# Kernel tuning notes

Measured on AMD Instinct MI355X. Metric: run time of the kernel, lower is better.

The kernel has to match this reference:

```python
import jax, jax.numpy as jnp
import numpy as np

N_NODES = 6890
N_ANGLES = 8
K_CHEB = 15
N_DESC = 544
HIDDEN = 64
N_CLASS = 6890
M = N_ANGLES * N_NODES  # 55120, size of anisotropic Laplacian
DEG = 16
NNZ = M * DEG
BN_EPS = 1e-5


def setup_inputs() -> dict:
    key = jax.random.key(0)
    ks = jax.random.split(key, 16)
    x = jax.random.normal(ks[0], (N_NODES, N_DESC), dtype=jnp.float32)
    # sparse anisotropic Laplacian (M x M), ~DEG nnz per row
    rows = jnp.repeat(jnp.arange(M, dtype=jnp.int32), DEG)
    cols = jax.random.randint(ks[1], (NNZ,), 0, M, dtype=jnp.int32)
    vals = jax.random.normal(ks[2], (NNZ,), dtype=jnp.float32) * 0.1
    # conv1: (K, n_angles*n_desc, 64); conv2..6 stacked: (5, K, n_angles*64, 64)
    def xavier(k, shape, fan_in, fan_out):
        lim = np.sqrt(6.0 / (fan_in + fan_out))
        return jax.random.uniform(k, shape, jnp.float32, -lim, lim)
    W1 = xavier(ks[3], (K_CHEB, N_ANGLES * N_DESC, HIDDEN), N_ANGLES * N_DESC, HIDDEN)
    Wc = xavier(ks[4], (5, K_CHEB, N_ANGLES * HIDDEN, HIDDEN), N_ANGLES * HIDDEN, HIDDEN)
    conv_b = jnp.zeros((6, HIDDEN), jnp.float32)
    bn_gamma = jnp.ones((6, HIDDEN), jnp.float32)
    bn_beta = jnp.zeros((6, HIDDEN), jnp.float32)
    fc2_w = xavier(ks[5], (HIDDEN, 256), HIDDEN, 256)
    fc2_b = jnp.zeros((256,), jnp.float32)
    fc3_w = xavier(ks[6], (256, N_CLASS), 256, N_CLASS)
    fc3_b = jnp.zeros((N_CLASS,), jnp.float32)
    return {"x": x, "rows": rows, "cols": cols, "vals": vals,
            "W1": W1, "Wc": Wc, "conv_b": conv_b,
            "bn_gamma": bn_gamma, "bn_beta": bn_beta,
            "fc2_w": fc2_w, "fc2_b": fc2_b, "fc3_w": fc3_w, "fc3_b": fc3_b}


def _spmm(rows, cols, vals, T):
    # (M x M sparse) @ (M x C) via gather + segment-sum
    return jax.ops.segment_sum(vals[:, None] * T[cols], rows, num_segments=M)


def _acs_conv(x, rows, cols, vals, W, b):
    # x: (N, C). Chebyshev recurrence on the (A*N, C) angle-stacked signal.
    N, C = x.shape
    A = N_ANGLES

    def proj(T, Wk):
        # (A*N, C) -> (N, A*C) @ (A*C, out)
        return T.reshape(A, N, C).transpose(1, 0, 2).reshape(N, A * C) @ Wk

    T0 = jnp.tile(x, (A, 1))
    out = proj(T0, W[0])
    T1 = _spmm(rows, cols, vals, T0)
    out = out + proj(T1, W[1])
    for k in range(2, K_CHEB):
        T2 = 2.0 * _spmm(rows, cols, vals, T1) - T0
        out = out + proj(T2, W[k])
        T0, T1 = T1, T2
    return out + b


def _bn_relu(x, gamma, beta):
    # BatchNorm1d (training-mode batch stats, biased variance) + ReLU
    mean = jnp.mean(x, axis=0)
    var = jnp.var(x, axis=0)
    return jax.nn.relu((x - mean) * jax.lax.rsqrt(var + BN_EPS) * gamma + beta)


def reference(x, rows, cols, vals, W1, Wc, conv_b, bn_gamma, bn_beta,
              fc2_w, fc2_b, fc3_w, fc3_b):
    h = _bn_relu(_acs_conv(x, rows, cols, vals, W1, conv_b[0]), bn_gamma[0], bn_beta[0])
    for i in range(5):
        h = _bn_relu(_acs_conv(h, rows, cols, vals, Wc[i], conv_b[i + 1]),
                     bn_gamma[i + 1], bn_beta[i + 1])
    h = jax.nn.relu(h @ fc2_w + fc2_b)
    # dropout is identity at inference
    return h @ fc3_w + fc3_b
```

## Files before the change

### kernel.cpp

```cpp
#include <hip/hip_runtime.h>
#include <cstdint>
#include <cstddef>

#define NN 6890
#define NA 8
#define KC 15
#define ND 544
#define MR (NA * NN)
#define DEG 16
#define NNZ (MR * DEG)
#define BN_EPS 1e-5f
#define NRG 108
#define PB (NA * NRG)

typedef unsigned int u32;
typedef _Float16 f16;
typedef __attribute__((ext_vector_type(8))) _Float16 f16x8;
typedef __attribute__((ext_vector_type(4))) float f32x4;

union U4H8 { uint4 q; f16 h[8]; f16x8 v; };

__device__ __forceinline__ u32 packh(float a, float b) {
    union { f16 h[2]; u32 u; } c;
    c.h[0] = (f16)a; c.h[1] = (f16)b; return c.u;
}
__device__ __forceinline__ uint4 pack8h(const float* t) {
    uint4 m;
    m.x = packh(t[0], t[1]); m.y = packh(t[2], t[3]);
    m.z = packh(t[4], t[5]); m.w = packh(t[6], t[7]);
    return m;
}
__device__ __forceinline__ void acc8h(float* s, float v, uint4 g) {
    U4H8 c; c.q = g;
    #pragma unroll
    for (int i = 0; i < 8; ++i) s[i] += v * (float)c.h[i];
}

__global__ __launch_bounds__(256)
void prep_cv_kernel(const int* __restrict__ cols, const float* __restrict__ vals,
                    uint4* __restrict__ cvq)
{
    const int q = blockIdx.x * 256 + threadIdx.x;
    if (q >= NNZ / 4) return;
    const int4   c = ((const int4*)cols)[q];
    const float4 v = ((const float4*)vals)[q];
    uint4 o;
    o.x = ((u32)c.x & 0xffffu) | ((u32)c.y << 16);
    o.y = ((u32)c.z & 0xffffu) | ((u32)c.w << 16);
    o.z = packh(v.x, v.y);
    o.w = packh(v.z, v.w);
    cvq[q] = o;
}

template<int CC>
__global__ __launch_bounds__(256)
void tile_slab_kernel(const float* __restrict__ X, int C_in, int c0,
                      uint4* __restrict__ slab0)
{
    constexpr int LPR = CC / 8;
    constexpr int RPB = 256 / LPR;
    const int tid = threadIdx.x;
    const int j = tid % LPR, rloc = tid / LPR;
    const int r = blockIdx.x * RPB + rloc;
    if (r >= MR) return;
    const int n = r % NN;
    const float* xp = X + (size_t)n * C_in + c0 + 8 * j;
    const float4 t0 = *(const float4*)xp;
    const float4 t1 = *(const float4*)(xp + 4);
    float t[8] = { t0.x, t0.y, t0.z, t0.w, t1.x, t1.y, t1.z, t1.w };
    slab0[(size_t)r * LPR + j] = pack8h(t);
}

template<int CC, bool CHEB>
__device__ __forceinline__
void spmm_body(const uint4* __restrict__ sp, const uint4* __restrict__ sc,
               uint4* __restrict__ sw, const uint4* __restrict__ cvq,
               uint4* cvl)
{
    constexpr int LPR = CC / 8;
    constexpr int RPB = 256 / LPR;
    const int tid = threadIdx.x;
    const int j = tid % LPR, rloc = tid / LPR;
    const int r0 = blockIdx.x * RPB;
    const int nrow = (MR - r0) < RPB ? (MR - r0) : RPB;
    for (int e = tid; e < nrow * 4; e += 256)
        cvl[e] = cvq[(size_t)r0 * 4 + e];
    __syncthreads();
    const int r = r0 + rloc;
    if (r >= MR) return;

    int c[16]; float v[16];
    #pragma unroll
    for (int q = 0; q < 4; ++q) {
        const uint4 cq = cvl[rloc * 4 + q];
        c[4 * q + 0] = cq.x & 0xffffu; c[4 * q + 1] = cq.x >> 16;
        c[4 * q + 2] = cq.y & 0xffffu; c[4 * q + 3] = cq.y >> 16;
        union { u32 u; f16 h[2]; } z, w_;
        z.u = cq.z; w_.u = cq.w;
        v[4 * q + 0] = (float)z.h[0]; v[4 * q + 1] = (float)z.h[1];
        v[4 * q + 2] = (float)w_.h[0]; v[4 * q + 3] = (float)w_.h[1];
    }
    float s[8] = {0.f, 0.f, 0.f, 0.f, 0.f, 0.f, 0.f, 0.f};
    #pragma unroll
    for (int d = 0; d < DEG; ++d)
        acc8h(s, v[d], sp[(size_t)c[d] * LPR + j]);
    float t[8];
    if (CHEB) {
        U4H8 p; p.q = sc[(size_t)r * LPR + j];
        #pragma unroll
        for (int i = 0; i < 8; ++i) t[i] = 2.f * s[i] - (float)p.h[i];
    } else {
        #pragma unroll
        for (int i = 0; i < 8; ++i) t[i] = s[i];
    }
    sw[(size_t)r * LPR + j] = pack8h(t);
}

template<int CC, bool CHEB>
__global__ __launch_bounds__(256)
void spmm_only_kernel(const uint4* __restrict__ sp, const uint4* __restrict__ sc,
                      uint4* __restrict__ sw, const uint4* __restrict__ cvq)
{
    constexpr int RPB = 256 / (CC / 8);
    __shared__ uint4 cvl[RPB * 4];
    spmm_body<CC, CHEB>(sp, sc, sw, cvq, cvl);
}

template<int SCC, int NPROJ, bool FIRSTP>
__device__ __forceinline__
void proj_body(int pb, const uint4* __restrict__ s0, const uint4* __restrict__ s1,
               const float* __restrict__ W, float* __restrict__ part,
               int C_in, int c0, int kbase, u32* WH, u32* WL)
{
    constexpr int LPRF   = SCC / 8;
    constexpr int SLICES = SCC >= 64 ? SCC / 64 : 1;
    constexpr int SCH    = SCC >= 64 ? 64 : SCC;
    constexpr int CCH    = SCH / 32;
    const int tid = threadIdx.x;
    const int l = tid & 63, w = tid >> 6;
    const int a = pb / NRG, rg = pb % NRG;
    const int rows0 = rg * 64;
    const int hi16 = l >> 4;

    const int arow = rows0 + w * 16 + (l & 15);
    const int arc  = arow < NN ? arow : NN - 1;
    const size_t abase = (size_t)(a * NN + arc) * LPRF;

    f32x4 acc[4];
    #pragma unroll
    for (int nt = 0; nt < 4; ++nt) {
        #pragma unroll
        for (int rr = 0; rr < 4; ++rr) {
            const int orow = rows0 + w * 16 + hi16 * 4 + rr;
            float vv = 0.f;
            if (!FIRSTP && orow < NN)
                vv = part[((size_t)a * NN + orow) * 64 + nt * 16 + (l & 15)];
            acc[nt][rr] = vv;
        }
    }

    #pragma unroll
    for (int p = 0; p < NPROJ; ++p) {
        const uint4* sl = (p == 0) ? s0 : s1;
        #pragma unroll
        for (int s = 0; s < SLICES; ++s) {
            const float* Wk = W + ((size_t)(kbase + p) * NA * C_in
                                   + (size_t)a * C_in + c0 + s * 64) * 64;
            if (p | s) __syncthreads();
            for (int e = tid; e < CCH * 1024; e += 256) {
                const int i2 = e & 3;
                const int ll = (e >> 2) & 63;
                const int nt = (e >> 8) & 3;
                const int h  = e >> 10;
                const int cc  = h * 32 + (ll >> 4) * 8 + 2 * i2;
                const int col = nt * 16 + (ll & 15);
                const float w0 = Wk[(size_t)cc * 64 + col];
                const float w1 = Wk[(size_t)(cc + 1) * 64 + col];
                const f16 h0 = (f16)w0, h1 = (f16)w1;
                union { f16 h[2]; u32 u; } ph, pl;
                ph.h[0] = h0; ph.h[1] = h1;
                pl.h[0] = (f16)(w0 - (float)h0); pl.h[1] = (f16)(w1 - (float)h1);
                WH[e] = ph.u; WL[e] = pl.u;
            }
            __syncthreads();
            #pragma unroll
            for (int h = 0; h < CCH; ++h) {
                U4H8 af; af.q = sl[abase + s * 8 + h * 4 + hi16];
                #pragma unroll
                for (int nt = 0; nt < 4; ++nt) {
                    const int be = ((h * 4 + nt) * 64 + l) * 4;
                    U4H8 bh, bl;
                    bh.q = *(const uint4*)&WH[be];
                    bl.q = *(const uint4*)&WL[be];
                    acc[nt] = __builtin_amdgcn_mfma_f32_16x16x32_f16(af.v, bh.v, acc[nt], 0, 0, 0);
                    acc[nt] = __builtin_amdgcn_mfma_f32_16x16x32_f16(af.v, bl.v, acc[nt], 0, 0, 0);
                }
            }
        }
    }

    #pragma unroll
    for (int nt = 0; nt < 4; ++nt) {
        #pragma unroll
        for (int rr = 0; rr < 4; ++rr) {
            const int orow = rows0 + w * 16 + hi16 * 4 + rr;
            if (orow < NN)
                part[((size_t)a * NN + orow) * 64 + nt * 16 + (l & 15)] = acc[nt][rr];
        }
    }
}

template<int CC, bool FIRSTP>
__global__ __launch_bounds__(256)
void step2_kernel(const uint4* __restrict__ sp, const uint4* __restrict__ sc,
                  uint4* __restrict__ sw, const uint4* __restrict__ cvq,
                  const float* __restrict__ W, float* __restrict__ part,
                  int C_in, int c0, int kbase, int NB)
{
    constexpr int RPB = 256 / (CC / 8);
    __shared__ uint4 cvl[RPB * 4];
    __shared__ u32 WH[2048];
    __shared__ u32 WL[2048];
    if ((int)blockIdx.x < NB)
        spmm_body<CC, true>(sp, sc, sw, cvq, cvl);
    else
        proj_body<CC, 2, FIRSTP>((int)blockIdx.x - NB, sc, sp, W, part, C_in, c0, kbase, WH, WL);
}

template<int CC>
__global__ __launch_bounds__(256)
void proj_final_kernel(const uint4* __restrict__ sl, const float* __restrict__ W,
                       float* __restrict__ part, int C_in, int c0, int kproj)
{
    __shared__ u32 WH[2048];
    __shared__ u32 WL[2048];
    proj_body<CC, 1, false>((int)blockIdx.x, sl, sl, W, part, C_in, c0, kproj, WH, WL);
}

__global__ void bn_reduce_kernel(const float* __restrict__ part, float* __restrict__ acc)
{
    const int e = blockIdx.x * blockDim.x + threadIdx.x;
    if (e >= NN * 64) return;
    float s = 0.f;
    #pragma unroll
    for (int a = 0; a < NA; ++a) s += part[(size_t)a * NN * 64 + e];
    acc[e] = s;
}

__global__ __launch_bounds__(256)
void bn_stats_kernel(const float* __restrict__ acc, const float* __restrict__ gamma,
                     const float* __restrict__ beta, float* __restrict__ bnp)
{
    const int h = blockIdx.x;
    float s = 0.f, sq = 0.f;
    for (int n = threadIdx.x; n < NN; n += 256) {
        const float v = acc[(size_t)n * 64 + h];
        s += v; sq += v * v;
    }
    __shared__ float ls[256], lq[256];
    ls[threadIdx.x] = s; lq[threadIdx.x] = sq;
    __syncthreads();
    for (int st = 128; st > 0; st >>= 1) {
        if (threadIdx.x < st) { ls[threadIdx.x] += ls[threadIdx.x + st]; lq[threadIdx.x] += lq[threadIdx.x + st]; }
        __syncthreads();
    }
    if (threadIdx.x == 0) {
        const float mean = ls[0] / (float)NN;
        const float var  = lq[0] / (float)NN - mean * mean;
        const float sc   = gamma[h] / sqrtf(var + BN_EPS);
        bnp[h]      = sc;
        bnp[64 + h] = beta[h] - mean * sc;
    }
}

__global__ void bn_apply_kernel(const float* __restrict__ acc, const float* __restrict__ bnp,
                                float* __restrict__ H)
{
    const int e = blockIdx.x * blockDim.x + threadIdx.x;
    if (e >= NN * 64) return;
    const int h = e & 63;
    const float v = acc[e] * bnp[h] + bnp[64 + h];
    H[e] = v > 0.f ? v : 0.f;
}

template<bool RELU>
__global__ __launch_bounds__(256)
void gemm_bias_kernel(const float* __restrict__ A, const float* __restrict__ B,
                      const float* __restrict__ bias, float* __restrict__ C,
                      int Mm, int Nn, int Kk)
{
    __shared__ float As[16][132];
    __shared__ float Bs[16][132];
    const int tx = threadIdx.x & 15, ty = threadIdx.x >> 4;
    const int m0 = blockIdx.y * 128, n0 = blockIdx.x * 128;
    const bool full = (m0 + 128 <= Mm) && (n0 + 128 <= Nn);
    float acc[8][8] = {};
    for (int k0 = 0; k0 < Kk; k0 += 16) {
        if (full) {
            #pragma unroll
            for (int e = threadIdx.x; e < 512; e += 256) {
                const int i = e >> 2, q = e & 3;
                const float4 a4 = *(const float4*)&A[(size_t)(m0 + i) * Kk + k0 + 4 * q];
                As[4 * q + 0][i] = a4.x; As[4 * q + 1][i] = a4.y;
                As[4 * q + 2][i] = a4.z; As[4 * q + 3][i] = a4.w;
            }
            #pragma unroll
            for (int e = threadIdx.x; e < 512; e += 256) {
                const int kk = e >> 5, q = e & 31;
                *(float4*)&Bs[kk][4 * q] = *(const float4*)&B[(size_t)(k0 + kk) * Nn + n0 + 4 * q];
            }
        } else {
            for (int e = threadIdx.x; e < 128 * 16; e += 256) {
                const int i = e >> 4, kk = e & 15;
                const int row = m0 + i;
                As[kk][i] = (row < Mm) ? A[(size_t)row * Kk + k0 + kk] : 0.f;
            }
            for (int e = threadIdx.x; e < 16 * 128; e += 256) {
                const int kk = e >> 7, jj = e & 127;
                const int col = n0 + jj;
                Bs[kk][jj] = (col < Nn) ? B[(size_t)(k0 + kk) * Nn + col] : 0.f;
            }
        }
        __syncthreads();
        #pragma unroll
        for (int kk = 0; kk < 16; ++kk) {
            float av[8], bv[8];
            *(float4*)&av[0] = *(const float4*)&As[kk][ty * 4];
            *(float4*)&av[4] = *(const float4*)&As[kk][64 + ty * 4];
            *(float4*)&bv[0] = *(const float4*)&Bs[kk][tx * 4];
            *(float4*)&bv[4] = *(const float4*)&Bs[kk][64 + tx * 4];
            #pragma unroll
            for (int i = 0; i < 8; ++i)
                #pragma unroll
                for (int jj = 0; jj < 8; ++jj)
                    acc[i][jj] += av[i] * bv[jj];
        }
        __syncthreads();
    }
    for (int i = 0; i < 8; ++i) {
        const int row = m0 + (i < 4 ? ty * 4 + i : 64 + ty * 4 + (i - 4));
        if (row >= Mm) continue;
        for (int jj = 0; jj < 8; ++jj) {
            const int col = n0 + (jj < 4 ? tx * 4 + jj : 64 + tx * 4 + (jj - 4));
            if (col >= Nn) continue;
            float v = acc[i][jj] + bias[col];
            if (RELU) v = fmaxf(v, 0.f);
            C[(size_t)row * Nn + col] = v;
        }
    }
}

__global__ __launch_bounds__(256)
void w3_split_kernel(const float* __restrict__ W, f16* __restrict__ Wh, f16* __restrict__ Wl)
{
    __shared__ float t[64][65];
    const int tid = threadIdx.x;
    const int n0 = blockIdx.x * 64, k0 = blockIdx.y * 64;
    for (int e = tid; e < 64 * 64; e += 256) {
        const int kk = e >> 6, nn = e & 63;
        const int gn = n0 + nn;
        t[kk][nn] = (gn < NN) ? W[(size_t)(k0 + kk) * NN + gn] : 0.f;
    }
    __syncthreads();
    for (int e = tid; e < 64 * 8; e += 256) {
        const int nn = e >> 3, c8 = e & 7;
        const int gn = n0 + nn;
        if (gn >= NN) continue;
        const size_t ob = ((size_t)((k0 >> 3) + c8) * NN + gn) * 8;
        f16 vh[8], vl[8];
        #pragma unroll
        for (int i = 0; i < 8; ++i) {
            const float w = t[c8 * 8 + i][nn];
            const f16 h = (f16)w;
            vh[i] = h; vl[i] = (f16)(w - (float)h);
        }
        *(uint4*)&Wh[ob] = *(const uint4*)vh;
        *(uint4*)&Wl[ob] = *(const uint4*)vl;
    }
}

__global__ __launch_bounds__(256)
void f2_split_kernel(const float* __restrict__ f2, f16* __restrict__ Ah, f16* __restrict__ Al)
{
    const int row = blockIdx.x * 256 + threadIdx.x;
    const int c = blockIdx.y;
    if (row >= NN) return;
    const float4 a0 = *(const float4*)&f2[(size_t)row * 256 + c * 8];
    const float4 a1 = *(const float4*)&f2[(size_t)row * 256 + c * 8 + 4];
    const float vv[8] = { a0.x, a0.y, a0.z, a0.w, a1.x, a1.y, a1.z, a1.w };
    f16 vh[8], vl[8];
    #pragma unroll
    for (int i = 0; i < 8; ++i) {
        const f16 h = (f16)vv[i];
        vh[i] = h; vl[i] = (f16)(vv[i] - (float)h);
    }
    const size_t ob = ((size_t)c * NN + row) * 8;
    *(uint4*)&Ah[ob] = *(const uint4*)vh;
    *(uint4*)&Al[ob] = *(const uint4*)vl;
}

__global__ __launch_bounds__(256)
void fc3_mfma_kernel(const f16* __restrict__ Ah, const f16* __restrict__ Al,
                     const f16* __restrict__ Bh, const f16* __restrict__ Bl,
                     const float* __restrict__ bias, float* __restrict__ C)
{
    const int tid = threadIdx.x, l = tid & 63, w = tid >> 6;
    const int wm = w >> 1, wn = w & 1, hi16 = l >> 4;
    const int m0 = blockIdx.y * 128, n0 = blockIdx.x * 128;

    size_t aoff[4], boff[4];
    #pragma unroll
    for (int mf = 0; mf < 4; ++mf) {
        int row = m0 + wm * 64 + mf * 16 + (l & 15);
        if (row > NN - 1) row = NN - 1;
        aoff[mf] = (size_t)row * 8;
    }
    #pragma unroll
    for (int nf = 0; nf < 4; ++nf) {
        int col = n0 + wn * 64 + nf * 16 + (l & 15);
        if (col > NN - 1) col = NN - 1;
        boff[nf] = (size_t)col * 8;
    }

    f32x4 acc[4][4];
    #pragma unroll
    for (int mf = 0; mf < 4; ++mf)
        #pragma unroll
        for (int nf = 0; nf < 4; ++nf)
            acc[mf][nf] = (f32x4){0.f, 0.f, 0.f, 0.f};

    for (int k0 = 0; k0 < 256; k0 += 32) {
        const size_t cb = (size_t)((k0 >> 3) + hi16) * NN * 8;
        f16x8 ah[4], al[4], bh[4], bl[4];
        #pragma unroll
        for (int mf = 0; mf < 4; ++mf) {
            ah[mf] = *(const f16x8*)(Ah + cb + aoff[mf]);
            al[mf] = *(const f16x8*)(Al + cb + aoff[mf]);
        }
        #pragma unroll
        for (int nf = 0; nf < 4; ++nf) {
            bh[nf] = *(const f16x8*)(Bh + cb + boff[nf]);
            bl[nf] = *(const f16x8*)(Bl + cb + boff[nf]);
        }
        #pragma unroll
        for (int mf = 0; mf < 4; ++mf)
            #pragma unroll
            for (int nf = 0; nf < 4; ++nf) {
                acc[mf][nf] = __builtin_amdgcn_mfma_f32_16x16x32_f16(ah[mf], bh[nf], acc[mf][nf], 0, 0, 0);
                acc[mf][nf] = __builtin_amdgcn_mfma_f32_16x16x32_f16(ah[mf], bl[nf], acc[mf][nf], 0, 0, 0);
                acc[mf][nf] = __builtin_amdgcn_mfma_f32_16x16x32_f16(al[mf], bh[nf], acc[mf][nf], 0, 0, 0);
            }
    }

    #pragma unroll
    for (int mf = 0; mf < 4; ++mf) {
        #pragma unroll
        for (int nf = 0; nf < 4; ++nf) {
            const int col = n0 + wn * 64 + nf * 16 + (l & 15);
            if (col >= NN) continue;
            const float bv = bias[col];
            #pragma unroll
            for (int rr = 0; rr < 4; ++rr) {
                const int row = m0 + wm * 64 + mf * 16 + hi16 * 4 + rr;
                if (row < NN)
                    C[(size_t)row * NN + col] = acc[mf][nf][rr] + bv;
            }
        }
    }
}

template<int CC>
static void run_chunk(bool first, const float* X, int C_in, int c0,
                      const uint4* cvq, const float* W,
                      uint4* slabs, float* part, hipStream_t stream)
{
    constexpr int RPB = 256 / (CC / 8);
    const int NB = (MR + RPB - 1) / RPB;
    const size_t SLOT = (size_t)MR * (CC / 8);
    uint4* sl[3] = { slabs, slabs + SLOT, slabs + 2 * SLOT };

    tile_slab_kernel<CC><<<NB, 256, 0, stream>>>(X, C_in, c0, sl[0]);
    spmm_only_kernel<CC, false><<<NB, 256, 0, stream>>>(sl[0], sl[0], sl[1], cvq);
    for (int k = 2; k < KC; ++k) {
        const int p = (k - 1) % 3, c = (k - 2) % 3, n = k % 3;
        if (k & 1) {
            spmm_only_kernel<CC, true><<<NB, 256, 0, stream>>>(sl[p], sl[c], sl[n], cvq);
        } else {
            if (first && k == 2)
                step2_kernel<CC, true ><<<NB + PB, 256, 0, stream>>>(
                    sl[p], sl[c], sl[n], cvq, W, part, C_in, c0, k - 2, NB);
            else
                step2_kernel<CC, false><<<NB + PB, 256, 0, stream>>>(
                    sl[p], sl[c], sl[n], cvq, W, part, C_in, c0, k - 2, NB);
        }
    }
    proj_final_kernel<CC><<<PB, 256, 0, stream>>>(sl[(KC - 1) % 3], W, part, C_in, c0, KC - 1);
}

extern "C" void kernel_launch(void* const* d_in, const int* in_sizes, int n_in,
                              void* d_out, int out_size, void* d_ws, size_t ws_size,
                              hipStream_t stream)
{
    (void)in_sizes; (void)n_in; (void)out_size;
    const float* x     = (const float*)d_in[0];
    const int*   cols  = (const int*)  d_in[2];
    const float* vals  = (const float*)d_in[3];
    const float* W1    = (const float*)d_in[4];
    const float* Wc    = (const float*)d_in[5];
    const float* gamma = (const float*)d_in[7];
    const float* beta  = (const float*)d_in[8];
    const float* fc2w  = (const float*)d_in[9];
    const float* fc2b  = (const float*)d_in[10];
    const float* fc3w  = (const float*)d_in[11];
    const float* fc3b  = (const float*)d_in[12];

    const size_t MT = (size_t)MR * 64;
    const size_t FIXED = (size_t)(NNZ / 4) * 16
                       + MT * 4
                       + (size_t)NN * 64 * 4 * 2
                       + (size_t)NN * 256 * 4
                       + (size_t)NN * 256 * 2 * 4
                       + 1024;
    const size_t ring256 = 3 * (size_t)MR * 512;
    const size_t ring128 = 3 * (size_t)MR * 256;
    const size_t ring64  = 3 * (size_t)MR * 128;
    int ccL0 = 64;
    size_t ring = ring64;
    if (ws_size >= FIXED + ring256)      { ccL0 = 256; ring = ring256; }
    else if (ws_size >= FIXED + ring128) { ccL0 = 128; ring = ring128; }

    char* base = (char*)d_ws;
    size_t off = 0;
    uint4* cvq  = (uint4*)(base + off); off += (size_t)(NNZ / 4) * 16;
    uint4* slabs = (uint4*)(base + off); off += ring;
    float* part = (float*)(base + off); off += MT * 4;
    float* acc  = (float*)(base + off); off += (size_t)NN * 64 * 4;
    float* H    = (float*)(base + off); off += (size_t)NN * 64 * 4;
    float* f2   = (float*)(base + off); off += (size_t)NN * 256 * 4;
    f16* f2h    = (f16*)(base + off);   off += (size_t)NN * 256 * 2;
    f16* f2l    = (f16*)(base + off);   off += (size_t)NN * 256 * 2;
    f16* W3h    = (f16*)(base + off);   off += (size_t)NN * 256 * 2;
    f16* W3l    = (f16*)(base + off);   off += (size_t)NN * 256 * 2;
    float* bnp  = (float*)(base + off);

    prep_cv_kernel<<<(NNZ / 4 + 255) / 256, 256, 0, stream>>>(cols, vals, cvq);
    w3_split_kernel<<<dim3(108, 4), 256, 0, stream>>>(fc3w, W3h, W3l);

    for (int li = 0; li < 6; ++li) {
        const int C_in = (li == 0) ? ND : 64;
        const float* X = (li == 0) ? x : H;
        const float* W = (li == 0) ? W1 : Wc + (size_t)(li - 1) * KC * (NA * 64) * 64;

        if (li == 0) {
            int c0 = 0;
            bool first = true;
            const int wide = ccL0;
            while (c0 + wide <= 512) {
                if (wide == 256)      run_chunk<256>(first, X, C_in, c0, cvq, W, slabs, part, stream);
                else if (wide == 128) run_chunk<128>(first, X, C_in, c0, cvq, W, slabs, part, stream);
                else                  run_chunk<64> (first, X, C_in, c0, cvq, W, slabs, part, stream);
                c0 += wide; first = false;
            }
            while (c0 + 64 <= ND) {
                run_chunk<64>(first, X, C_in, c0, cvq, W, slabs, part, stream);
                c0 += 64; first = false;
            }
            run_chunk<32>(false, X, C_in, c0, cvq, W, slabs, part, stream);
        } else {
            run_chunk<64>(true, X, C_in, 0, cvq, W, slabs, part, stream);
        }

        bn_reduce_kernel<<<(NN * 64 + 255) / 256, 256, 0, stream>>>(part, acc);
        bn_stats_kernel<<<64, 256, 0, stream>>>(acc, gamma + li * 64, beta + li * 64, bnp);
        bn_apply_kernel<<<(NN * 64 + 255) / 256, 256, 0, stream>>>(acc, bnp, H);
    }

    gemm_bias_kernel<true><<<dim3(2, 54), 256, 0, stream>>>(H, fc2w, fc2b, f2, NN, 256, 64);
    f2_split_kernel<<<dim3(27, 32), 256, 0, stream>>>(f2, f2h, f2l);
    fc3_mfma_kernel<<<dim3(54, 54), 256, 0, stream>>>(f2h, f2l, W3h, W3l, fc3b, (float*)d_out);
}
```

Baseline: 4.172 ms.

## Fuse BN-ReLU into slab tiling and use output buffer as slab ring

Applies the BatchNorm scale/shift and ReLU inside the slab-tiling kernel for layers 2-6, so the separate bn_apply pass runs only after the last layer. The Chebyshev slab ring now lives in the output buffer, which lets layer 1 always use 256-wide channel chunks (two 256 chunks plus a 32 remainder) regardless of workspace size. This removes one elementwise kernel and its memory traffic per layer and gives fewer, wider chunks in the first layer. It relies on the output buffer being large enough to hold the ring and being fully overwritten by the final fc3 kernel.

```diff
diff --git a/kernel.cpp b/kernel.cpp
--- a/kernel.cpp
+++ b/kernel.cpp
@@ -52,10 +52,10 @@
     cvq[q] = o;
 }
 
-template<int CC>
+template<int CC, bool BN>
 __global__ __launch_bounds__(256)
 void tile_slab_kernel(const float* __restrict__ X, int C_in, int c0,
-                      uint4* __restrict__ slab0)
+                      uint4* __restrict__ slab0, const float* __restrict__ bnp)
 {
     constexpr int LPR = CC / 8;
     constexpr int RPB = 256 / LPR;
@@ -68,6 +68,14 @@
     const float4 t0 = *(const float4*)xp;
     const float4 t1 = *(const float4*)(xp + 4);
     float t[8] = { t0.x, t0.y, t0.z, t0.w, t1.x, t1.y, t1.z, t1.w };
+    if (BN) {
+        const int ch = c0 + 8 * j;
+        #pragma unroll
+        for (int i = 0; i < 8; ++i) {
+            const float v = t[i] * bnp[ch + i] + bnp[64 + ch + i];
+            t[i] = v > 0.f ? v : 0.f;
+        }
+    }
     slab0[(size_t)r * LPR + j] = pack8h(t);
 }
 
@@ -469,9 +477,9 @@
     }
 }
 
-template<int CC>
+template<int CC, bool BN>
 static void run_chunk(bool first, const float* X, int C_in, int c0,
-                      const uint4* cvq, const float* W,
+                      const uint4* cvq, const float* W, const float* bnp,
                       uint4* slabs, float* part, hipStream_t stream)
 {
     constexpr int RPB = 256 / (CC / 8);
@@ -479,7 +487,7 @@
     const size_t SLOT = (size_t)MR * (CC / 8);
     uint4* sl[3] = { slabs, slabs + SLOT, slabs + 2 * SLOT };
 
-    tile_slab_kernel<CC><<<NB, 256, 0, stream>>>(X, C_in, c0, sl[0]);
+    tile_slab_kernel<CC, BN><<<NB, 256, 0, stream>>>(X, C_in, c0, sl[0], bnp);
     spmm_only_kernel<CC, false><<<NB, 256, 0, stream>>>(sl[0], sl[0], sl[1], cvq);
     for (int k = 2; k < KC; ++k) {
         const int p = (k - 1) % 3, c = (k - 2) % 3, n = k % 3;
@@ -501,7 +509,7 @@
                               void* d_out, int out_size, void* d_ws, size_t ws_size,
                               hipStream_t stream)
 {
-    (void)in_sizes; (void)n_in; (void)out_size;
+    (void)in_sizes; (void)n_in; (void)out_size; (void)ws_size;
     const float* x     = (const float*)d_in[0];
     const int*   cols  = (const int*)  d_in[2];
     const float* vals  = (const float*)d_in[3];
@@ -515,24 +523,12 @@
     const float* fc3b  = (const float*)d_in[12];
 
     const size_t MT = (size_t)MR * 64;
-    const size_t FIXED = (size_t)(NNZ / 4) * 16
-                       + MT * 4
-                       + (size_t)NN * 64 * 4 * 2
-                       + (size_t)NN * 256 * 4
-                       + (size_t)NN * 256 * 2 * 4
-                       + 1024;
-    const size_t ring256 = 3 * (size_t)MR * 512;
-    const size_t ring128 = 3 * (size_t)MR * 256;
-    const size_t ring64  = 3 * (size_t)MR * 128;
-    int ccL0 = 64;
-    size_t ring = ring64;
-    if (ws_size >= FIXED + ring256)      { ccL0 = 256; ring = ring256; }
-    else if (ws_size >= FIXED + ring128) { ccL0 = 128; ring = ring128; }
+
+    uint4* slabs = (uint4*)d_out;
 
     char* base = (char*)d_ws;
     size_t off = 0;
     uint4* cvq  = (uint4*)(base + off); off += (size_t)(NNZ / 4) * 16;
-    uint4* slabs = (uint4*)(base + off); off += ring;
     float* part = (float*)(base + off); off += MT * 4;
     float* acc  = (float*)(base + off); off += (size_t)NN * 64 * 4;
     float* H    = (float*)(base + off); off += (size_t)NN * 64 * 4;
@@ -548,31 +544,20 @@
 
     for (int li = 0; li < 6; ++li) {
         const int C_in = (li == 0) ? ND : 64;
-        const float* X = (li == 0) ? x : H;
         const float* W = (li == 0) ? W1 : Wc + (size_t)(li - 1) * KC * (NA * 64) * 64;
 
         if (li == 0) {
-            int c0 = 0;
-            bool first = true;
-            const int wide = ccL0;
-            while (c0 + wide <= 512) {
-                if (wide == 256)      run_chunk<256>(first, X, C_in, c0, cvq, W, slabs, part, stream);
-                else if (wide == 128) run_chunk<128>(first, X, C_in, c0, cvq, W, slabs, part, stream);
-                else                  run_chunk<64> (first, X, C_in, c0, cvq, W, slabs, part, stream);
-                c0 += wide; first = false;
-            }
-            while (c0 + 64 <= ND) {
-                run_chunk<64>(first, X, C_in, c0, cvq, W, slabs, part, stream);
-                c0 += 64; first = false;
-            }
-            run_chunk<32>(false, X, C_in, c0, cvq, W, slabs, part, stream);
+            run_chunk<256, false>(true,  x, C_in, 0,   cvq, W, nullptr, slabs, part, stream);
+            run_chunk<256, false>(false, x, C_in, 256, cvq, W, nullptr, slabs, part, stream);
+            run_chunk<32,  false>(false, x, C_in, 512, cvq, W, nullptr, slabs, part, stream);
         } else {
-            run_chunk<64>(true, X, C_in, 0, cvq, W, slabs, part, stream);
+            run_chunk<64, true>(true, acc, C_in, 0, cvq, W, bnp, slabs, part, stream);
         }
 
         bn_reduce_kernel<<<(NN * 64 + 255) / 256, 256, 0, stream>>>(part, acc);
         bn_stats_kernel<<<64, 256, 0, stream>>>(acc, gamma + li * 64, beta + li * 64, bnp);
-        bn_apply_kernel<<<(NN * 64 + 255) / 256, 256, 0, stream>>>(acc, bnp, H);
+        if (li == 5)
+            bn_apply_kernel<<<(NN * 64 + 255) / 256, 256, 0, stream>>>(acc, bnp, H);
     }
 
     gemm_bias_kernel<true><<<dim3(2, 54), 256, 0, stream>>>(H, fc2w, fc2b, f2, NN, 256, 64);
```

After: 4.085 ms. 1.02x faster.
